# Performance work log

Hardware: AMD Instinct MI355X
Metric: run time of the kernel (lower is better)

## Reference

```python
import jax, jax.numpy as jnp
import numpy as np

EMB = 512          # embedding_size
N_NODES = 16384    # len(nodes)
N_EVENTS = 1_000_000
N_PAIRS = 200_000  # distinct (variant, place) groups


def setup_inputs() -> dict:
    key = jax.random.key(0)
    rng = np.random.default_rng(0)
    embeddings = jax.random.normal(key, (N_NODES, EMB), dtype=jnp.float32)
    pair_place = rng.integers(0, N_NODES, N_PAIRS, dtype=np.int32)   # place id per (variant,place) pair
    event_pair = rng.integers(0, N_PAIRS, N_EVENTS, dtype=np.int32)  # which pair each event belongs to
    event_src = rng.integers(0, N_NODES, N_EVENTS, dtype=np.int32)   # source activity per event
    event_ndst = rng.integers(1, 5, N_EVENTS, dtype=np.int32)        # |next_activities| per event (>=1)
    dst_event = np.repeat(np.arange(N_EVENTS, dtype=np.int32), event_ndst)  # event id per dst entry
    dst_node = rng.integers(0, N_NODES, dst_event.shape[0], dtype=np.int32) # dst activity node ids
    return {
        "embeddings": embeddings,
        "pair_place": jnp.asarray(pair_place),
        "event_pair": jnp.asarray(event_pair),
        "event_src": jnp.asarray(event_src),
        "event_ndst": jnp.asarray(event_ndst),
        "dst_event": jnp.asarray(dst_event),
        "dst_node": jnp.asarray(dst_node),
    }


def reference(embeddings, pair_place, event_pair, event_src, event_ndst, dst_event, dst_node):
    N, E = embeddings.shape
    num_events = event_pair.shape[0]
    num_pairs = pair_place.shape[0]
    # torch.mean(torch.stack(e)) averages over ALL elements of the stacked
    # [k, 1, 3E] concat tensors, so only per-row means of the embeddings matter:
    # mean(cat(place_f, src_f, dst_f)) = (mean(place_f)+mean(src_f)+mean(dst_f))/3.
    node_mean = embeddings.mean(axis=1)  # [N]
    # dst_f = (sum over next_activities of embeddings[dst]) / (n_dst + 1)
    dst_sum = jax.ops.segment_sum(node_mean[dst_node], dst_event, num_segments=num_events)  # [num_events]
    ndst = event_ndst.astype(node_mean.dtype)
    event_place = pair_place[event_pair]
    # per-event scalar = mean over the 3E concat features
    s = (node_mean[event_place] + node_mean[event_src] + dst_sum / (ndst + 1.0)) / 3.0
    # per (variant, place) pair: mean over that pair's events
    pair_sum = jax.ops.segment_sum(s, event_pair, num_segments=num_pairs)
    pair_cnt = jax.ops.segment_sum(jnp.ones_like(s), event_pair, num_segments=num_pairs)
    pair_mean = jnp.where(pair_cnt > 0, pair_sum / jnp.maximum(pair_cnt, 1.0), 0.0)
    # per place: mean over the pairs that touched it (only pairs with >=1 event exist)
    place_sum = jax.ops.segment_sum(pair_mean, pair_place, num_segments=N)
    place_cnt = jax.ops.segment_sum(jnp.where(pair_cnt > 0, 1.0, 0.0).astype(s.dtype), pair_place, num_segments=N)
    place_mean = jnp.where(place_cnt > 0, place_sum / jnp.maximum(place_cnt, 1.0), 0.0)
    # final row is the scalar broadcast across cat_embedding_size = 3*E columns
    return jnp.broadcast_to(place_mean[:, None], (N, 3 * E))
```

## Files before the change

### kernel.cpp

```cpp
#include <hip/hip_runtime.h>
#include <hip/hip_fp16.h>

constexpr int EMB = 512;

typedef float floatx4 __attribute__((ext_vector_type(4)));

constexpr float T_SCALE = 1048576.0f;
constexpr float T_INV_SCALE = 1.0f / 1048576.0f;

__device__ __forceinline__ unsigned pack1_32(float t) {
    int q = __float2int_rn(t * T_SCALE);
    return (unsigned)(q + (1 << 26));
}
__device__ __forceinline__ void unpack32(unsigned a, int& cnt, float& sum) {
    cnt = (int)((a + (1u << 25)) >> 26);
    int q = (int)(a - ((unsigned)cnt << 26));
    sum = (float)q * T_INV_SCALE;
}

constexpr float FP_SCALE = 4194304.0f;
constexpr float FP_INV_SCALE = 1.0f / 4194304.0f;

__device__ __forceinline__ unsigned long long pack1_64(float v) {
    long long q = (long long)__float2int_rn(v * FP_SCALE);
    return (unsigned long long)(q + (1LL << 32));
}
__device__ __forceinline__ void unpack64(unsigned long long p, int& cnt, float& sum) {
    long long t = (long long)p;
    cnt = (int)((t + (1LL << 31)) >> 32);
    long long q = t - ((long long)cnt << 32);
    sum = (float)q * FP_INV_SCALE;
}

__global__ void node_mean_k(const float* __restrict__ emb,
                            float* __restrict__ node_mean,
                            __half* __restrict__ node_mean16, int n_nodes) {
    int gwave = (blockIdx.x * blockDim.x + threadIdx.x) >> 6;
    int lane = threadIdx.x & 63;
    if (gwave >= n_nodes) return;
    const float4* row = (const float4*)emb + (size_t)gwave * (EMB / 4);
    float4 a = row[lane];
    float4 b = row[lane + 64];
    float s = (a.x + a.y) + (a.z + a.w) + (b.x + b.y) + (b.z + b.w);
#pragma unroll
    for (int off = 32; off > 0; off >>= 1)
        s += __shfl_down(s, off, 64);
    if (lane == 0) {
        float m = s * (1.0f / (float)EMB);
        node_mean[gwave] = m;
        node_mean16[gwave] = __float2half(m);
    }
}

__global__ void event_fused_k(const int* __restrict__ dst_event,
                              const int* __restrict__ dst_node,
                              const int* __restrict__ event_pair,
                              const int* __restrict__ event_src,
                              const __half* __restrict__ nm16,
                              unsigned* __restrict__ pair_acc, int n_dst) {
    int i = blockIdx.x * blockDim.x + threadIdx.x;
    if (i >= n_dst) return;
    int e = dst_event[i];
    if (i > 0 && dst_event[i - 1] == e) return;
    float dsum = __half2float(nm16[dst_node[i]]);
    int nd = 1;
    int j = i + 1;
    while (j < n_dst && dst_event[j] == e) {
        dsum += __half2float(nm16[dst_node[j]]);
        ++nd; ++j;
    }
    float t = __half2float(nm16[event_src[e]]) + dsum / (float)(nd + 1);
    atomicAdd(&pair_acc[event_pair[e]], pack1_32(t));
}

__global__ void pair_k(const unsigned* __restrict__ pair_acc,
                       const int* __restrict__ pair_place,
                       const float* __restrict__ node_mean,
                       unsigned long long* __restrict__ place_acc, int n_pairs) {
    int p = blockIdx.x * blockDim.x + threadIdx.x;
    if (p >= n_pairs) return;
    int cnt; float tsum;
    unpack32(pair_acc[p], cnt, tsum);
    if (cnt > 0) {
        int pl = pair_place[p];
        float pm = node_mean[pl] * (1.0f / 3.0f) + tsum / (3.0f * (float)cnt);
        atomicAdd(&place_acc[pl], pack1_64(pm));
    }
}

__global__ void out_k(const unsigned long long* __restrict__ place_acc,
                      float* __restrict__ out, int n_float4) {
    constexpr int ROW_F4 = 3 * EMB / 4;
    int stride = gridDim.x * blockDim.x;
    for (int g = blockIdx.x * blockDim.x + threadIdx.x; g < n_float4; g += stride) {
        int row = (int)((unsigned)g / (unsigned)ROW_F4);
        int cnt; float psum;
        unpack64(place_acc[row], cnt, psum);
        float v = (cnt > 0) ? psum / (float)cnt : 0.0f;
        floatx4 val = {v, v, v, v};
        __builtin_nontemporal_store(val, (floatx4*)out + g);
    }
}

extern "C" void kernel_launch(void* const* d_in, const int* in_sizes, int n_in,
                              void* d_out, int out_size, void* d_ws, size_t ws_size,
                              hipStream_t stream) {
    const float* emb        = (const float*)d_in[0];
    const int*   pair_place = (const int*)d_in[1];
    const int*   event_pair = (const int*)d_in[2];
    const int*   event_src  = (const int*)d_in[3];
    const int*   dst_event  = (const int*)d_in[5];
    const int*   dst_node   = (const int*)d_in[6];

    const int n_nodes  = in_sizes[0] / EMB;
    const int n_pairs  = in_sizes[1];
    const int n_dst    = in_sizes[5];

    char* base = (char*)d_ws;
    float* node_mean = (float*)base;
    __half* nm16 = (__half*)(base + (size_t)n_nodes * 4);
    unsigned* pair_acc = (unsigned*)(base + (size_t)n_nodes * 6);
    unsigned long long* place_acc =
        (unsigned long long*)(base + (size_t)n_nodes * 6 + (size_t)n_pairs * 4);

    (void)hipMemsetAsync(pair_acc, 0, (size_t)n_pairs * 4 + (size_t)n_nodes * 8, stream);

    node_mean_k<<<(n_nodes + 3) / 4, 256, 0, stream>>>(emb, node_mean, nm16, n_nodes);
    event_fused_k<<<(n_dst + 255) / 256, 256, 0, stream>>>(
        dst_event, dst_node, event_pair, event_src, nm16, pair_acc, n_dst);
    pair_k<<<(n_pairs + 255) / 256, 256, 0, stream>>>(
        pair_acc, pair_place, node_mean, place_acc, n_pairs);
    const int n_float4 = n_nodes * (3 * EMB / 4);
    out_k<<<4096, 256, 0, stream>>>(place_acc, (float*)d_out, n_float4);
}
```

Baseline: 222.1 us.

## Fuse accumulator zeroing into node-mean kernel, prefetch event gathers, per-row output blocks

The separate memset is dropped; the node-mean kernel now also zeroes the pair and place accumulators, saving a launch. The event kernel loads up to four following dst entries and their half-precision means up front with predication, so the dependent gathers overlap instead of running one by one in a loop. The output kernel uses one block per row, so the per-element division by the row width and the grid-stride loop go away. The cost is more speculative loads in the event kernel and many more small blocks in the output kernel.

Result: faster. 217.2 us (-2.2%).

```diff
diff --git a/kernel.cpp b/kernel.cpp
--- a/kernel.cpp
+++ b/kernel.cpp
@@ -4,6 +4,7 @@
 constexpr int EMB = 512;
 
 typedef float floatx4 __attribute__((ext_vector_type(4)));
+typedef unsigned uintx4 __attribute__((ext_vector_type(4)));
 
 constexpr float T_SCALE = 1048576.0f;
 constexpr float T_INV_SCALE = 1.0f / 1048576.0f;
@@ -34,8 +35,12 @@
 
 __global__ void node_mean_k(const float* __restrict__ emb,
                             float* __restrict__ node_mean,
-                            __half* __restrict__ node_mean16, int n_nodes) {
-    int gwave = (blockIdx.x * blockDim.x + threadIdx.x) >> 6;
+                            __half* __restrict__ node_mean16,
+                            uintx4* __restrict__ zero4, int n_zero4,
+                            int n_nodes) {
+    int g = blockIdx.x * blockDim.x + threadIdx.x;
+    if (g < n_zero4) zero4[g] = (uintx4){0u, 0u, 0u, 0u};
+    int gwave = g >> 6;
     int lane = threadIdx.x & 63;
     if (gwave >= n_nodes) return;
     const float4* row = (const float4*)emb + (size_t)gwave * (EMB / 4);
@@ -62,15 +67,31 @@
     if (i >= n_dst) return;
     int e = dst_event[i];
     if (i > 0 && dst_event[i - 1] == e) return;
-    float dsum = __half2float(nm16[dst_node[i]]);
-    int nd = 1;
-    int j = i + 1;
-    while (j < n_dst && dst_event[j] == e) {
+    int j1 = i + 1, j2 = i + 2, j3 = i + 3;
+    bool b1 = j1 < n_dst, b2 = j2 < n_dst, b3 = j3 < n_dst;
+    int e1 = b1 ? dst_event[j1] : -1;
+    int e2 = b2 ? dst_event[j2] : -1;
+    int e3 = b3 ? dst_event[j3] : -1;
+    int d0 = dst_node[i];
+    int d1 = b1 ? dst_node[j1] : 0;
+    int d2 = b2 ? dst_node[j2] : 0;
+    int d3 = b3 ? dst_node[j3] : 0;
+    int pr = event_pair[e];
+    float sv = __half2float(nm16[event_src[e]]);
+    float h0 = __half2float(nm16[d0]);
+    float h1 = __half2float(nm16[d1]);
+    float h2 = __half2float(nm16[d2]);
+    float h3 = __half2float(nm16[d3]);
+    bool v1 = (e1 == e), v2 = (e2 == e), v3 = (e3 == e);
+    float dsum = h0 + (v1 ? h1 : 0.0f) + (v2 ? h2 : 0.0f) + (v3 ? h3 : 0.0f);
+    int nd = 1 + (int)v1 + (int)v2 + (int)v3;
+    int j = i + 4;
+    while (v3 && j < n_dst && dst_event[j] == e) {
         dsum += __half2float(nm16[dst_node[j]]);
         ++nd; ++j;
     }
-    float t = __half2float(nm16[event_src[e]]) + dsum / (float)(nd + 1);
-    atomicAdd(&pair_acc[event_pair[e]], pack1_32(t));
+    float t = sv + dsum / (float)(nd + 1);
+    atomicAdd(&pair_acc[pr], pack1_32(t));
 }
 
 __global__ void pair_k(const unsigned* __restrict__ pair_acc,
@@ -89,17 +110,18 @@
 }
 
 __global__ void out_k(const unsigned long long* __restrict__ place_acc,
-                      float* __restrict__ out, int n_float4) {
+                      float* __restrict__ out) {
     constexpr int ROW_F4 = 3 * EMB / 4;
-    int stride = gridDim.x * blockDim.x;
-    for (int g = blockIdx.x * blockDim.x + threadIdx.x; g < n_float4; g += stride) {
-        int row = (int)((unsigned)g / (unsigned)ROW_F4);
-        int cnt; float psum;
-        unpack64(place_acc[row], cnt, psum);
-        float v = (cnt > 0) ? psum / (float)cnt : 0.0f;
-        floatx4 val = {v, v, v, v};
-        __builtin_nontemporal_store(val, (floatx4*)out + g);
-    }
+    int row = blockIdx.x;
+    int t = threadIdx.x;
+    int cnt; float psum;
+    unpack64(place_acc[row], cnt, psum);
+    float v = (cnt > 0) ? psum / (float)cnt : 0.0f;
+    floatx4 val = {v, v, v, v};
+    floatx4* dst = (floatx4*)out + (size_t)row * ROW_F4;
+    __builtin_nontemporal_store(val, dst + t);
+    if (t < ROW_F4 - 256)
+        __builtin_nontemporal_store(val, dst + 256 + t);
 }
 
 extern "C" void kernel_launch(void* const* d_in, const int* in_sizes, int n_in,
@@ -123,13 +145,13 @@
     unsigned long long* place_acc =
         (unsigned long long*)(base + (size_t)n_nodes * 6 + (size_t)n_pairs * 4);
 
-    (void)hipMemsetAsync(pair_acc, 0, (size_t)n_pairs * 4 + (size_t)n_nodes * 8, stream);
+    const int n_zero4 = (n_pairs * 4 + n_nodes * 8 + 15) / 16;
 
-    node_mean_k<<<(n_nodes + 3) / 4, 256, 0, stream>>>(emb, node_mean, nm16, n_nodes);
+    node_mean_k<<<(n_nodes + 3) / 4, 256, 0, stream>>>(
+        emb, node_mean, nm16, (uintx4*)pair_acc, n_zero4, n_nodes);
     event_fused_k<<<(n_dst + 255) / 256, 256, 0, stream>>>(
         dst_event, dst_node, event_pair, event_src, nm16, pair_acc, n_dst);
     pair_k<<<(n_pairs + 255) / 256, 256, 0, stream>>>(
         pair_acc, pair_place, node_mean, place_acc, n_pairs);
-    const int n_float4 = n_nodes * (3 * EMB / 4);
-    out_k<<<4096, 256, 0, stream>>>(place_acc, (float*)d_out, n_float4);
+    out_k<<<n_nodes, 256, 0, stream>>>(place_acc, (float*)d_out);
 }
```
